# Performance work log

Hardware: AMD Instinct MI355X
Metric: run time of the kernel (lower is better)

## Reference

```python
import jax, jax.numpy as jnp
import numpy as np

B, N, F = 8, 2048, 128
H1, H2, D1 = 32, 64, 128


def setup_inputs() -> dict:
    key = jax.random.key(0)
    ks = jax.random.split(key, 10)
    x = jax.random.normal(ks[0], (B, N, F), dtype=jnp.float32)
    a = jax.random.uniform(ks[1], (B, N, N), dtype=jnp.float32)
    # GCN layer kernels (glorot-ish scale) and biases
    W1 = jax.random.normal(ks[2], (F, H1), dtype=jnp.float32) * (1.0 / np.sqrt(F))
    b1 = jnp.zeros((H1,), dtype=jnp.float32)
    W2 = jax.random.normal(ks[3], (H1, H2), dtype=jnp.float32) * (1.0 / np.sqrt(H1))
    b2 = jnp.zeros((H2,), dtype=jnp.float32)
    # Dense classifier after flatten: input dim = N * H2
    Wd = jax.random.normal(ks[4], (N * H2, D1), dtype=jnp.float32) * (1.0 / np.sqrt(N * H2))
    bd = jnp.zeros((D1,), dtype=jnp.float32)
    Wo = jax.random.normal(ks[5], (D1, 1), dtype=jnp.float32) * (1.0 / np.sqrt(D1))
    bo = jnp.zeros((1,), dtype=jnp.float32)
    return {"x": x, "a": a, "W1": W1, "b1": b1, "W2": W2, "b2": b2,
            "Wd": Wd, "bd": bd, "Wo": Wo, "bo": bo}


def reference(x, a, W1, b1, W2, b2, Wd, bd, Wo, bo):
    # GCNConv 1: relu(A @ (X @ W1) + b1)   [B,N,F] -> [B,N,H1]
    h = jax.nn.relu(jnp.einsum('bnm,bmh->bnh', a, x @ W1) + b1)
    # GCNConv 2: relu(A @ (H @ W2) + b2)   -> [B,N,H2]
    h = jax.nn.relu(jnp.einsum('bnm,bmh->bnh', a, h @ W2) + b2)
    # Flatten -> Dense(128, relu) -> (Dropout is identity at inference) -> Dense(1, sigmoid)
    h = h.reshape(h.shape[0], -1)          # [B, N*H2]
    h = jax.nn.relu(h @ Wd + bd)           # [B, D1]
    return jax.nn.sigmoid(h @ Wo + bo)     # [B, 1]
```

## Files before the change

kernel.cpp:

```cpp
#include <hip/hip_runtime.h>
#include <math.h>

#define B_  8
#define N_  2048
#define F_  128
#define H1_ 32
#define H2_ 64
#define D1_ 128
#define KS_ 8
#define KSEG_ (N_ / KS_)

typedef unsigned short u16;
typedef unsigned int   u32;
typedef __attribute__((ext_vector_type(8))) short short8;
typedef __attribute__((ext_vector_type(4))) float f32x4;

__device__ __forceinline__ u32 rne2(float e0, float e1) {
  u32 u0 = __float_as_uint(e0), u1 = __float_as_uint(e1);
  u0 = (u0 + 0x7FFFu + ((u0 >> 16) & 1u)) >> 16;
  u1 = (u1 + 0x7FFFu + ((u1 >> 16) & 1u)) & 0xFFFF0000u;
  return u0 | u1;
}
__device__ __forceinline__ uint4 rne8(const float4 a, const float4 b) {
  return make_uint4(rne2(a.x, a.y), rne2(a.z, a.w), rne2(b.x, b.y), rne2(b.z, b.w));
}

template<int H, int LDST>
__device__ __forceinline__ void pack_frags(const float* s, int b, int cgbase,
                                           u16* __restrict__ oh, int tid) {
  constexpr int CGRP = H / 16;
  constexpr int PASSES = H * 8 / 256;
#pragma unroll
  for (int p = 0; p < PASSES; ++p) {
    int q = tid + p * 256;
    int h = q >> 3, nn = (q & 7) * 8;
    u32 hw[4];
#pragma unroll
    for (int j = 0; j < 4; ++j)
      hw[j] = rne2(s[(nn + 2 * j) * LDST + h], s[(nn + 2 * j + 1) * LDST + h]);
    int ch = h >> 4, cl = h & 15;
    int cg = cgbase + (nn >> 5);
    int lanep = ((nn >> 3) & 3) * 16 + cl;
    size_t o = ((((size_t)b * CGRP + ch) * (N_ / 32) + cg) * 64 + lanep) * 8;
    *(uint4*)(oh + o) = make_uint4(hw[0], hw[1], hw[2], hw[3]);
  }
}

__global__ __launch_bounds__(256) void k_xw1cvt(const float* __restrict__ x,
                                                const float* __restrict__ W1,
                                                u16* __restrict__ oh) {
  __shared__ float xs[64][F_];
  __shared__ float w1s[F_ * H1_];
  __shared__ float s[64][H1_ + 1];
  const int b = blockIdx.y;
  const int n0 = blockIdx.x * 64;
  const int tid = threadIdx.x;
  const float* xp = x + ((size_t)b * N_ + n0) * F_;
#pragma unroll
  for (int i = 0; i < 8; ++i) {
    int q = tid + i * 256;
    int r = q >> 5, c4 = (q & 31) * 4;
    *(float4*)&xs[r][c4] = *(const float4*)(xp + (size_t)r * F_ + c4);
  }
#pragma unroll
  for (int i = 0; i < 4; ++i)
    ((float4*)w1s)[tid + i * 256] = ((const float4*)W1)[tid + i * 256];
  __syncthreads();
  const int r = tid >> 2, c0 = (tid & 3) * 8;
  float acc[8] = {};
#pragma unroll
  for (int k = 0; k < F_; ++k) {
    float xv = xs[r][k];
#pragma unroll
    for (int j = 0; j < 8; ++j)
      acc[j] = fmaf(xv, w1s[k * H1_ + c0 + j], acc[j]);
  }
#pragma unroll
  for (int j = 0; j < 8; ++j) s[r][c0 + j] = acc[j];
  __syncthreads();
  pack_frags<H1_, H1_ + 1>(&s[0][0], b, blockIdx.x * 2, oh, tid);
}

__global__ __launch_bounds__(256) void k_l1fuse(const float* __restrict__ P1,
                                                const float* __restrict__ b1,
                                                const float* __restrict__ W2,
                                                u16* __restrict__ oh) {
  __shared__ float h1s[64][H1_ + 1];
  __shared__ float w2s[H1_ * H2_];
  __shared__ float hw2s[64][H2_ + 1];
  const int b = blockIdx.y;
  const int n0 = blockIdx.x * 64;
  const int tid = threadIdx.x;
  constexpr size_t TOT = (size_t)B_ * N_ * H1_;
#pragma unroll
  for (int i = 0; i < 2; ++i) {
    int q = tid + i * 256;
    int r = q >> 3, h4 = (q & 7) * 4;
    size_t base = (((size_t)b * N_) + n0 + r) * H1_ + h4;
    float4 bv = *(const float4*)(b1 + h4);
    float a0 = bv.x, a1 = bv.y, a2 = bv.z, a3 = bv.w;
#pragma unroll
    for (int zz = 0; zz < KS_; ++zz) {
      float4 v = *(const float4*)(P1 + base + (size_t)zz * TOT);
      a0 += v.x; a1 += v.y; a2 += v.z; a3 += v.w;
    }
    h1s[r][h4 + 0] = fmaxf(a0, 0.f);
    h1s[r][h4 + 1] = fmaxf(a1, 0.f);
    h1s[r][h4 + 2] = fmaxf(a2, 0.f);
    h1s[r][h4 + 3] = fmaxf(a3, 0.f);
  }
#pragma unroll
  for (int i = 0; i < 2; ++i)
    ((float4*)w2s)[tid + i * 256] = ((const float4*)W2)[tid + i * 256];
  __syncthreads();
  const int r = tid >> 2, c0 = (tid & 3) * 16;
  float acc[16] = {};
#pragma unroll
  for (int k = 0; k < H1_; ++k) {
    float hv = h1s[r][k];
#pragma unroll
    for (int j = 0; j < 16; ++j)
      acc[j] = fmaf(hv, w2s[k * H2_ + c0 + j], acc[j]);
  }
#pragma unroll
  for (int j = 0; j < 16; ++j) hw2s[r][c0 + j] = acc[j];
  __syncthreads();
  pack_frags<H2_, H2_ + 1>(&hw2s[0][0], b, blockIdx.x * 2, oh, tid);
}

template<int H>
__global__ __launch_bounds__(256, 6) void k_agemm_mfma(const float* __restrict__ A,
                                                       const u16* __restrict__ Bph,
                                                       float* __restrict__ P) {
  constexpr int NT = H / 16;
  constexpr int BK = 64;
  constexpr int NTILE = KSEG_ / BK;
  __shared__ u16 at[2][64][72];

  const int batch = blockIdx.y;
  const int z = blockIdx.z;
  const int m0 = blockIdx.x * 64;
  const int tid = threadIdx.x;
  const int lane = tid & 63;
  const int wave = tid >> 6;

  const float* Ab = A + (size_t)batch * N_ * N_ + (size_t)m0 * N_ + (size_t)z * KSEG_;
  const int srow = tid >> 2, sc0 = (tid & 3) * 16;

  const size_t cg0 = (size_t)z * (KSEG_ / 32);
  const u16* bhb = Bph + ((size_t)batch * NT) * (N_ / 32) * 512 + (size_t)lane * 8;

  float4 st[4];
#pragma unroll
  for (int i = 0; i < 4; ++i)
    st[i] = *(const float4*)(Ab + (size_t)srow * N_ + sc0 + 4 * i);
  *(uint4*)&at[0][srow][sc0]     = rne8(st[0], st[1]);
  *(uint4*)&at[0][srow][sc0 + 8] = rne8(st[2], st[3]);
  __syncthreads();

  f32x4 acc[NT];
#pragma unroll
  for (int c = 0; c < NT; ++c) acc[c] = (f32x4){0.f, 0.f, 0.f, 0.f};

  for (int t = 0; t < NTILE; ++t) {
    const int kk = t * BK;
    const int buf = t & 1;
    if (t + 1 < NTILE) {
#pragma unroll
      for (int i = 0; i < 4; ++i)
        st[i] = *(const float4*)(Ab + (size_t)srow * N_ + (kk + BK) + sc0 + 4 * i);
      __builtin_amdgcn_sched_barrier(0);
    }
#pragma unroll
    for (int c = 0; c < 2; ++c) {
      short8 av = *(const short8*)&at[buf][wave * 16 + (lane & 15)][c * 32 + (lane >> 4) * 8];
      const size_t co = (cg0 + (kk >> 5) + c) * 512;
#pragma unroll
      for (int ch = 0; ch < NT; ++ch) {
        union { short8 s; uint4 u; } bh;
        bh.u = *(const uint4*)(bhb + ((size_t)ch * (N_ / 32)) * 512 + co);
        acc[ch] = __builtin_amdgcn_mfma_f32_16x16x32_bf16(av, bh.s, acc[ch], 0, 0, 0);
      }
    }
    if (t + 1 < NTILE) {
      *(uint4*)&at[buf ^ 1][srow][sc0]     = rne8(st[0], st[1]);
      *(uint4*)&at[buf ^ 1][srow][sc0 + 8] = rne8(st[2], st[3]);
    }
    __syncthreads();
  }
  const int orow = m0 + wave * 16 + ((lane >> 4) << 2);
  float* pp = P + ((size_t)(z * B_ + batch) * N_ + orow) * H + (lane & 15);
#pragma unroll
  for (int ch = 0; ch < NT; ++ch)
#pragma unroll
    for (int j = 0; j < 4; ++j)
      pp[(size_t)j * H + ch * 16] = acc[ch][j];
}

__global__ __launch_bounds__(512) void k_densefuse(const float* __restrict__ P2,
                                                   const float* __restrict__ b2,
                                                   const float* __restrict__ Wd,
                                                   float* __restrict__ part) {
  constexpr int KC = 512;
  __shared__ float hs[B_][KC];
  __shared__ float psum[B_][D1_];
  const int kc0 = blockIdx.x * KC;
  const int n0 = blockIdx.x * 8;
  const int tid = threadIdx.x;
  constexpr size_t TOT = (size_t)B_ * N_ * H2_;
#pragma unroll
  for (int i = 0; i < 2; ++i) {
    int q = tid + i * 512;
    int b = q >> 7, k4 = (q & 127) * 4;
    int nl = k4 >> 6, h = k4 & 63;
    size_t base = (((size_t)b * N_) + n0 + nl) * H2_ + h;
    float4 bv = *(const float4*)(b2 + h);
    float a0 = bv.x, a1 = bv.y, a2 = bv.z, a3 = bv.w;
#pragma unroll
    for (int zz = 0; zz < KS_; ++zz) {
      float4 v = *(const float4*)(P2 + base + (size_t)zz * TOT);
      a0 += v.x; a1 += v.y; a2 += v.z; a3 += v.w;
    }
    hs[b][k4 + 0] = fmaxf(a0, 0.f);
    hs[b][k4 + 1] = fmaxf(a1, 0.f);
    hs[b][k4 + 2] = fmaxf(a2, 0.f);
    hs[b][k4 + 3] = fmaxf(a3, 0.f);
  }
  __syncthreads();
  const int d0 = (tid & 31) * 4;
  const int b  = (tid >> 5) & 7;
  const int ks = tid >> 8;
  float a0 = 0.f, a1 = 0.f, a2 = 0.f, a3 = 0.f;
  const float* wp = Wd + ((size_t)kc0 + ks * 256) * D1_ + d0;
  const float* hp = &hs[b][ks * 256];
#pragma unroll 4
  for (int k = 0; k < 256; ++k) {
    float4 w = *(const float4*)(wp + (size_t)k * D1_);
    float h = hp[k];
    a0 = fmaf(h, w.x, a0); a1 = fmaf(h, w.y, a1);
    a2 = fmaf(h, w.z, a2); a3 = fmaf(h, w.w, a3);
  }
  if (ks == 1) {
    psum[b][d0] = a0; psum[b][d0 + 1] = a1; psum[b][d0 + 2] = a2; psum[b][d0 + 3] = a3;
  }
  __syncthreads();
  if (ks == 0) {
    float* pp = part + ((size_t)blockIdx.x * B_ + b) * D1_ + d0;
    *(float4*)pp = make_float4(a0 + psum[b][d0], a1 + psum[b][d0 + 1],
                               a2 + psum[b][d0 + 2], a3 + psum[b][d0 + 3]);
  }
}

__global__ __launch_bounds__(1024) void k_dense_final(const float* __restrict__ part,
                                                      const float* __restrict__ bd,
                                                      const float* __restrict__ Wo,
                                                      const float* __restrict__ bo,
                                                      float* __restrict__ out) {
  __shared__ float hd[B_ * D1_];
  const int tid = threadIdx.x;
  float s = 0.f;
  for (int i = 0; i < 256; ++i) s += part[(size_t)i * (B_ * D1_) + tid];
  hd[tid] = fmaxf(s + bd[tid & (D1_ - 1)], 0.f);
  __syncthreads();
  if (tid < 512) {
    int w = tid >> 6, l = tid & 63;
    float v = hd[w * D1_ + l] * Wo[l] + hd[w * D1_ + 64 + l] * Wo[64 + l];
#pragma unroll
    for (int off = 32; off; off >>= 1) v += __shfl_down(v, off, 64);
    if (l == 0) out[w] = 1.f / (1.f + expf(-(v + bo[0])));
  }
}

extern "C" void kernel_launch(void* const* d_in, const int* in_sizes, int n_in,
                              void* d_out, int out_size, void* d_ws, size_t ws_size,
                              hipStream_t stream) {
  const float* x  = (const float*)d_in[0];
  const float* a  = (const float*)d_in[1];
  const float* W1 = (const float*)d_in[2];
  const float* b1 = (const float*)d_in[3];
  const float* W2 = (const float*)d_in[4];
  const float* b2 = (const float*)d_in[5];
  const float* Wd = (const float*)d_in[6];
  const float* bd = (const float*)d_in[7];
  const float* Wo = (const float*)d_in[8];
  const float* bo = (const float*)d_in[9];
  float* out = (float*)d_out;

  float* ws    = (float*)d_ws;
  float* P     = ws;
  u16*   Bt1h  = (u16*)(ws + 8388608);
  u16*   Bt2h  = (u16*)(ws + 8650752);
  float* dpart = ws + 9175040;

  k_xw1cvt<<<dim3(N_ / 64, B_), 256, 0, stream>>>(x, W1, Bt1h);
  k_agemm_mfma<H1_><<<dim3(N_ / 64, B_, KS_), 256, 0, stream>>>(a, Bt1h, P);
  k_l1fuse<<<dim3(N_ / 64, B_), 256, 0, stream>>>(P, b1, W2, Bt2h);
  k_agemm_mfma<H2_><<<dim3(N_ / 64, B_, KS_), 256, 0, stream>>>(a, Bt2h, P);
  k_densefuse<<<(N_ * H2_) / 512, 512, 0, stream>>>(P, b2, Wd, dpart);
  k_dense_final<<<1, 1024, 0, stream>>>(dpart, bd, Wo, bo, out);
}
```

Before: 113.6 us.

## Stage B fragments in shared memory and halve the split-K factor

Result: faster. 103.6 us (-8.8%).

```diff
diff --git a/kernel.cpp b/kernel.cpp
--- a/kernel.cpp
+++ b/kernel.cpp
@@ -7,7 +7,7 @@
 #define H1_ 32
 #define H2_ 64
 #define D1_ 128
-#define KS_ 8
+#define KS_ 4
 #define KSEG_ (N_ / KS_)
 
 typedef unsigned short u16;
@@ -129,13 +129,16 @@
 }
 
 template<int H>
-__global__ __launch_bounds__(256, 6) void k_agemm_mfma(const float* __restrict__ A,
+__global__ __launch_bounds__(256, 4) void k_agemm_mfma(const float* __restrict__ A,
                                                        const u16* __restrict__ Bph,
                                                        float* __restrict__ P) {
   constexpr int NT = H / 16;
   constexpr int BK = 64;
   constexpr int NTILE = KSEG_ / BK;
+  constexpr int CHSTR = (N_ / 32) * 512;
+  constexpr int BL = NT / 2;
   __shared__ u16 at[2][64][72];
+  __shared__ u16 bt[2][2][NT][64][8];
 
   const int batch = blockIdx.y;
   const int z = blockIdx.z;
@@ -147,15 +150,29 @@
   const float* Ab = A + (size_t)batch * N_ * N_ + (size_t)m0 * N_ + (size_t)z * KSEG_;
   const int srow = tid >> 2, sc0 = (tid & 3) * 16;
 
-  const size_t cg0 = (size_t)z * (KSEG_ / 32);
-  const u16* bhb = Bph + ((size_t)batch * NT) * (N_ / 32) * 512 + (size_t)lane * 8;
-
-  float4 st[4];
+  const int cg0 = z * (KSEG_ / 32);
+  const u16* Bb = Bph + (size_t)batch * NT * CHSTR;
+
+  float4 sa[4];
+  uint4  sb[BL];
+
 #pragma unroll
   for (int i = 0; i < 4; ++i)
-    st[i] = *(const float4*)(Ab + (size_t)srow * N_ + sc0 + 4 * i);
-  *(uint4*)&at[0][srow][sc0]     = rne8(st[0], st[1]);
-  *(uint4*)&at[0][srow][sc0 + 8] = rne8(st[2], st[3]);
+    sa[i] = *(const float4*)(Ab + (size_t)srow * N_ + sc0 + 4 * i);
+#pragma unroll
+  for (int i = 0; i < BL; ++i) {
+    int q = tid + i * 256, seg = q >> 6, l2 = q & 63;
+    int cc = seg / NT, ch = seg % NT;
+    sb[i] = *(const uint4*)(Bb + (size_t)ch * CHSTR + (size_t)(cg0 + cc) * 512 + l2 * 8);
+  }
+  *(uint4*)&at[0][srow][sc0]     = rne8(sa[0], sa[1]);
+  *(uint4*)&at[0][srow][sc0 + 8] = rne8(sa[2], sa[3]);
+#pragma unroll
+  for (int i = 0; i < BL; ++i) {
+    int q = tid + i * 256, seg = q >> 6, l2 = q & 63;
+    int cc = seg / NT, ch = seg % NT;
+    *(uint4*)&bt[0][cc][ch][l2][0] = sb[i];
+  }
   __syncthreads();
 
   f32x4 acc[NT];
@@ -163,28 +180,39 @@
   for (int c = 0; c < NT; ++c) acc[c] = (f32x4){0.f, 0.f, 0.f, 0.f};
 
   for (int t = 0; t < NTILE; ++t) {
-    const int kk = t * BK;
     const int buf = t & 1;
     if (t + 1 < NTILE) {
+      const int kk1 = (t + 1) * BK;
 #pragma unroll
       for (int i = 0; i < 4; ++i)
-        st[i] = *(const float4*)(Ab + (size_t)srow * N_ + (kk + BK) + sc0 + 4 * i);
+        sa[i] = *(const float4*)(Ab + (size_t)srow * N_ + kk1 + sc0 + 4 * i);
+#pragma unroll
+      for (int i = 0; i < BL; ++i) {
+        int q = tid + i * 256, seg = q >> 6, l2 = q & 63;
+        int cc = seg / NT, ch = seg % NT;
+        sb[i] = *(const uint4*)(Bb + (size_t)ch * CHSTR
+                                + (size_t)(cg0 + 2 * (t + 1) + cc) * 512 + l2 * 8);
+      }
       __builtin_amdgcn_sched_barrier(0);
     }
 #pragma unroll
     for (int c = 0; c < 2; ++c) {
       short8 av = *(const short8*)&at[buf][wave * 16 + (lane & 15)][c * 32 + (lane >> 4) * 8];
-      const size_t co = (cg0 + (kk >> 5) + c) * 512;
 #pragma unroll
       for (int ch = 0; ch < NT; ++ch) {
-        union { short8 s; uint4 u; } bh;
-        bh.u = *(const uint4*)(bhb + ((size_t)ch * (N_ / 32)) * 512 + co);
-        acc[ch] = __builtin_amdgcn_mfma_f32_16x16x32_bf16(av, bh.s, acc[ch], 0, 0, 0);
+        short8 bv = *(const short8*)&bt[buf][c][ch][lane][0];
+        acc[ch] = __builtin_amdgcn_mfma_f32_16x16x32_bf16(av, bv, acc[ch], 0, 0, 0);
       }
     }
     if (t + 1 < NTILE) {
-      *(uint4*)&at[buf ^ 1][srow][sc0]     = rne8(st[0], st[1]);
-      *(uint4*)&at[buf ^ 1][srow][sc0 + 8] = rne8(st[2], st[3]);
+      *(uint4*)&at[buf ^ 1][srow][sc0]     = rne8(sa[0], sa[1]);
+      *(uint4*)&at[buf ^ 1][srow][sc0 + 8] = rne8(sa[2], sa[3]);
+#pragma unroll
+      for (int i = 0; i < BL; ++i) {
+        int q = tid + i * 256, seg = q >> 6, l2 = q & 63;
+        int cc = seg / NT, ch = seg % NT;
+        *(uint4*)&bt[buf ^ 1][cc][ch][l2][0] = sb[i];
+      }
     }
     __syncthreads();
   }
@@ -288,9 +316,9 @@
 
   float* ws    = (float*)d_ws;
   float* P     = ws;
-  u16*   Bt1h  = (u16*)(ws + 8388608);
-  u16*   Bt2h  = (u16*)(ws + 8650752);
-  float* dpart = ws + 9175040;
+  u16*   Bt1h  = (u16*)(ws + 4194304);
+  u16*   Bt2h  = (u16*)(ws + 4456448);
+  float* dpart = ws + 4980736;
 
   k_xw1cvt<<<dim3(N_ / 64, B_), 256, 0, stream>>>(x, W1, Bt1h);
   k_agemm_mfma<H1_><<<dim3(N_ / 64, B_, KS_), 256, 0, stream>>>(a, Bt1h, P);
```
